# Optimization experiments

Measured on AMD Instinct MI355X. Metric: run time of the kernel, lower is better.

## Reference

```python
import jax, jax.numpy as jnp
import numpy as np

SCAD_A = 3.7
PERCENTILE_Q = 0.75
EPS = 1e-8
LAM_HAT = 0.9
PROP_STEP = 4


def setup_inputs() -> dict:
    key = jax.random.key(0)
    ks = jax.random.split(key, 4)
    N, IN, H, OUT = 4096, 512, 256, 64
    p = 32.0 / N  # avg degree ~32 (pre-symmetrization ~64 after OR, still sparse)
    u = jax.random.uniform(ks[0], (N, N))
    Au = u < p
    Asym = Au | Au.T
    eye = jnp.eye(N, dtype=bool)
    A = jnp.where(eye, 0.0, Asym.astype(jnp.float32))  # zero diagonal; add_loops adds I
    X = jax.random.normal(ks[1], (N, IN), dtype=jnp.float32)
    W1 = jax.random.normal(ks[2], (IN, H), dtype=jnp.float32) / np.sqrt(IN)
    b1 = jnp.zeros((H,), dtype=jnp.float32)
    W2 = jax.random.normal(ks[3], (H, OUT), dtype=jnp.float32) / np.sqrt(H)
    b2 = jnp.zeros((OUT,), dtype=jnp.float32)
    log_gamma_0 = jnp.asarray(np.log(3.0), dtype=jnp.float32)
    raw_decay = jnp.asarray(np.log(0.85 / 0.15), dtype=jnp.float32)
    raw_alpha_blend = jnp.asarray(0.0, dtype=jnp.float32)  # sigmoid -> 0.5 blend
    return {"A": A, "X": X, "W1": W1, "b1": b1, "W2": W2, "b2": b2,
            "log_gamma_0": log_gamma_0, "raw_decay": raw_decay,
            "raw_alpha_blend": raw_alpha_blend}


def _scad_weight(y, lam, a):
    # SCAD-derived reweighting: 1 for y<=lam, (a*lam - y)/((a-1)*y) in the middle, 0 beyond a*lam.
    y_safe = jnp.maximum(y, EPS)  # avoid inf/nan in unselected branch (forward value unchanged)
    w_mid = (a * lam - y) / ((a - 1.0) * y_safe)
    return jnp.where(y <= lam, 1.0, jnp.where(y <= a * lam, w_mid, 0.0))


def reference(A, X, W1, b1, W2, b2, log_gamma_0, raw_decay, raw_alpha_blend):
    N = A.shape[0]
    eye = jnp.eye(N, dtype=A.dtype)
    Ahat = A + eye                          # add_loops
    D = Ahat.sum(-1)                        # [N]
    D_sq = jnp.sqrt(D)[:, None]             # [N,1]
    A_tilde = Ahat / (D_sq * D_sq.T)        # sym_norm: D^{-1/2} A D^{-1/2}
    edge_mask = (Ahat > 0) & (eye == 0)     # A_bool & ~I
    has_edges = edge_mask.sum() > 0

    # MLP (eval mode: dropout inactive)
    F0 = jnp.maximum(X @ W1 + b1, 0.0) @ W2 + b2   # [N, out_dim]

    alpha = jax.nn.sigmoid(raw_alpha_blend)
    g0 = jnp.exp(log_gamma_0)
    r = jax.nn.sigmoid(raw_decay)
    lam = 1.0 / LAM_HAT - 1.0

    Fc = F0
    for k in range(PROP_STEP):
        gamma_param_k = g0 * (r ** k)
        Fn = Fc / D_sq
        nrm = jnp.linalg.norm(Fn, axis=-1, keepdims=True)
        Fu = Fn / jnp.maximum(nrm, EPS)     # F.normalize semantics
        y = jnp.clip(1.0 - Fu @ Fu.T, 0.0, 2.0)  # [N,N] cosine distance
        y = jax.lax.stop_gradient(y)        # y.detach()
        y_edges = jnp.where(edge_mask, y, jnp.nan)
        gamma_data_k = jnp.nanquantile(y_edges, PERCENTILE_Q)
        gamma_data_k = jnp.maximum(jnp.where(has_edges, gamma_data_k, 1.0), EPS)
        lam_combined = alpha * (gamma_param_k / SCAD_A) + (1.0 - alpha) * (gamma_data_k / SCAD_A)
        W = _scad_weight(y, lam_combined, SCAD_A)
        W = W * (1.0 - eye)
        W = jnp.where(jnp.isnan(W), 1.0, W)
        Q_hat = ((W * Ahat).sum(-1) / D + lam)[:, None]
        Fc = (W * A_tilde) @ Fc / Q_hat + lam * F0 / Q_hat
    return Fc
```

## Files before the change

### kernel.cpp

```cpp
#include <hip/hip_runtime.h>
#include <hip/hip_cooperative_groups.h>
#include <math.h>

namespace cg = cooperative_groups;

#define N_NODES 4096
#define IN_DIM  512
#define H_DIM   256
#define OUT_DIM 64
#define SCAD_Af 3.7f
#define EPSf    1e-8f
#define NBINS   2048
#define MAXD    256
#define KSPLIT  4
#define KS_MG   2

__device__ __forceinline__ float scad_w(float y, float lamc) {
    if (y <= lamc) return 1.0f;
    if (y <= SCAD_Af * lamc)
        return (SCAD_Af * lamc - y) / ((SCAD_Af - 1.0f) * fmaxf(y, EPSf));
    return 0.0f;
}

__global__ __launch_bounds__(256, 4)
void k_mega(const float* __restrict__ A,  const float* __restrict__ X,
            const float* __restrict__ W1, const float* __restrict__ b1,
            const float* __restrict__ W2, const float* __restrict__ b2,
            const float* __restrict__ lg0, const float* __restrict__ rdec,
            const float* __restrict__ ralpha,
            int* __restrict__ colIdx, int* __restrict__ rowcnt,
            float* __restrict__ D, float* __restrict__ isD,
            float* __restrict__ Fu, float* __restrict__ part,
            float* __restrict__ F0, float* __restrict__ FcA,
            float* __restrict__ FcB, float* __restrict__ outp,
            unsigned int* __restrict__ hist01) {
    cg::grid_group grid = cg::this_grid();
    const int tid = threadIdx.x;
    const int blk = blockIdx.x;
    const int gid = blk * 256 + tid;
    const int w = tid >> 6, lane = tid & 63;

    __shared__ union {
        struct { float As[16][68]; float Bs[16][64]; } g;
        unsigned int hl[NBINS];
        unsigned int psum[256];
        struct { float h[4][H_DIM]; float w2[64][64]; } m;
    } sm;
    __shared__ float y_loc[4][MAXD];
    __shared__ float vv[2];
    __shared__ float sh_scal;
    __shared__ int   sh_nE;
    __shared__ int   cnt4[4];

    if (blk < 512) {
        int bz = blk >> 8, rem = blk & 255;
        int bx = rem & 3, by = rem >> 2;
        int tx = tid & 15, ty = tid >> 4;
        int bm = by * 64, bn = bx * 64;
        int kbeg = bz * (IN_DIM / KS_MG);
        float acc[4][4] = {};
        for (int k0 = kbeg; k0 < kbeg + IN_DIM / KS_MG; k0 += 16) {
            {
                int r = tid >> 2, kv = tid & 3;
                float4 v = *(const float4*)(X + (size_t)(bm + r) * IN_DIM + k0 + kv * 4);
                sm.g.As[kv * 4 + 0][r] = v.x;
                sm.g.As[kv * 4 + 1][r] = v.y;
                sm.g.As[kv * 4 + 2][r] = v.z;
                sm.g.As[kv * 4 + 3][r] = v.w;
            }
            {
                int kk = tid >> 4, nv = tid & 15;
                *(float4*)&sm.g.Bs[kk][nv * 4] =
                    *(const float4*)(W1 + (size_t)(k0 + kk) * H_DIM + bn + nv * 4);
            }
            __syncthreads();
#pragma unroll
            for (int kk = 0; kk < 16; kk++) {
                float a[4], b[4];
#pragma unroll
                for (int u = 0; u < 4; u++) { a[u] = sm.g.As[kk][ty * 4 + u]; b[u] = sm.g.Bs[kk][tx * 4 + u]; }
#pragma unroll
                for (int u = 0; u < 4; u++)
#pragma unroll
                    for (int v = 0; v < 4; v++) acc[u][v] += a[u] * b[v];
            }
            __syncthreads();
        }
        float* Cm = part + (size_t)bz * N_NODES * H_DIM;
#pragma unroll
        for (int u = 0; u < 4; u++) {
            int m2 = bm + ty * 4 + u;
#pragma unroll
            for (int v = 0; v < 4; v++)
                Cm[(size_t)m2 * H_DIM + bn + tx * 4 + v] = acc[u][v];
        }
    } else {
        int bb = blk - 512;
        int gid2 = bb * 256 + tid;
        if (gid2 < 2 * NBINS) hist01[gid2] = 0u;
#pragma unroll
        for (int rr = 0; rr < 2; rr++) {
            int i = bb * 8 + rr * 4 + w;
            if (lane == 0) cnt4[w] = 0;
            const float4* row4 = (const float4*)(A + (size_t)i * N_NODES);
            int* ci = colIdx + i * MAXD;
            for (int v = lane; v < N_NODES / 4; v += 64) {
                float4 x = row4[v];
                int j0 = v * 4;
                if (x.x != 0.0f) { int p = atomicAdd(&cnt4[w], 1); ci[p] = j0; }
                if (x.y != 0.0f) { int p = atomicAdd(&cnt4[w], 1); ci[p] = j0 + 1; }
                if (x.z != 0.0f) { int p = atomicAdd(&cnt4[w], 1); ci[p] = j0 + 2; }
                if (x.w != 0.0f) { int p = atomicAdd(&cnt4[w], 1); ci[p] = j0 + 3; }
            }
            if (lane == 0) {
                int t = cnt4[w];
                rowcnt[i] = t;
                float d = (float)t + 1.0f;
                D[i] = d;
                isD[i] = 1.0f / sqrtf(d);
            }
        }
    }
    grid.sync();

    {
        unsigned int s = 0;
        for (int q = tid; q < N_NODES; q += 256) s += (unsigned int)rowcnt[q];
        sm.psum[tid] = s;
        __syncthreads();
        for (int off = 128; off; off >>= 1) {
            if (tid < off) sm.psum[tid] += sm.psum[tid + off];
            __syncthreads();
        }
        if (tid == 0) sh_nE = (int)sm.psum[0];
        __syncthreads();

        int i = blk * 4 + w;
        const size_t tot = (size_t)N_NODES * H_DIM;
        const float* p0 = part + (size_t)i * H_DIM;
#pragma unroll
        for (int q = 0; q < 4; q++) {
            int k = q * 64 + lane;
            float s2 = p0[k] + p0[tot + k] + b1[k];
            sm.m.h[w][k] = fmaxf(s2, 0.0f);
        }
        float a0 = 0, a1 = 0, a2 = 0, a3 = 0;
        for (int k0 = 0; k0 < H_DIM; k0 += 64) {
            __syncthreads();
            const float4* src = (const float4*)(W2 + (size_t)k0 * OUT_DIM);
#pragma unroll
            for (int q = 0; q < 4; q++)
                ((float4*)sm.m.w2)[q * 256 + tid] = src[q * 256 + tid];
            __syncthreads();
#pragma unroll 16
            for (int kk = 0; kk < 64; kk += 4) {
                a0 += sm.m.h[w][k0 + kk + 0] * sm.m.w2[kk + 0][lane];
                a1 += sm.m.h[w][k0 + kk + 1] * sm.m.w2[kk + 1][lane];
                a2 += sm.m.h[w][k0 + kk + 2] * sm.m.w2[kk + 2][lane];
                a3 += sm.m.h[w][k0 + kk + 3] * sm.m.w2[kk + 3][lane];
            }
        }
        float f0 = (a0 + a1) + (a2 + a3) + b2[lane];
        F0[(size_t)i * 64 + lane] = f0;
        float fn = f0 * isD[i];
        float s2 = fn * fn;
        for (int off = 32; off; off >>= 1) s2 += __shfl_xor(s2, off, 64);
        Fu[(size_t)i * 64 + lane] = fn / fmaxf(sqrtf(s2), EPSf);
    }
    grid.sync();

    const float lam = (float)(1.0 / 0.9 - 1.0);
    const int eg = lane >> 2, el = lane & 3;
    const int i = blk * 4 + w, c = lane;
    const float* fin = F0;
    for (int k = 0; k < 4; k++) {
        float* fout = (k == 0) ? FcA : (k == 1) ? FcB : (k == 2) ? FcA : outp;
        unsigned int* histK    = hist01 + (k & 1) * NBINS;
        unsigned int* histNext = hist01 + ((k + 1) & 1) * NBINS;

        for (int b = tid; b < NBINS; b += 256) sm.hl[b] = 0u;
        __syncthreads();
        {
            int deg = rowcnt[i];
            const float4* Fu4 = (const float4*)Fu;
            float4 fi0 = Fu4[i * 16 + el * 4 + 0];
            float4 fi1 = Fu4[i * 16 + el * 4 + 1];
            float4 fi2 = Fu4[i * 16 + el * 4 + 2];
            float4 fi3 = Fu4[i * 16 + el * 4 + 3];
            for (int base = 0; base < deg; base += 16) {
                int e = base + eg;
                bool act = e < deg;
                int j = act ? colIdx[i * MAXD + e] : i;
                float4 a0 = Fu4[(size_t)j * 16 + el * 4 + 0];
                float4 a1 = Fu4[(size_t)j * 16 + el * 4 + 1];
                float4 a2 = Fu4[(size_t)j * 16 + el * 4 + 2];
                float4 a3 = Fu4[(size_t)j * 16 + el * 4 + 3];
                float s = fi0.x * a0.x + fi0.y * a0.y + fi0.z * a0.z + fi0.w * a0.w
                        + fi1.x * a1.x + fi1.y * a1.y + fi1.z * a1.z + fi1.w * a1.w
                        + fi2.x * a2.x + fi2.y * a2.y + fi2.z * a2.z + fi2.w * a2.w
                        + fi3.x * a3.x + fi3.y * a3.y + fi3.z * a3.z + fi3.w * a3.w;
                s += __shfl_xor(s, 1, 64);
                s += __shfl_xor(s, 2, 64);
                if (act && el == 0) {
                    float y = 1.0f - s;
                    y = fminf(fmaxf(y, 0.0f), 2.0f);
                    y_loc[w][e] = y;
                    int bin = (int)(y * (NBINS * 0.5f));
                    if (bin > NBINS - 1) bin = NBINS - 1;
                    atomicAdd(&sm.hl[bin], 1u);
                }
            }
        }
        __syncthreads();
        for (int b = tid; b < NBINS; b += 256) {
            unsigned int v = sm.hl[b];
            if (v) atomicAdd(&histK[b], v);
        }
        if (tid < 4 && blk * 4 + tid < NBINS) {}
        if (gid < NBINS) histNext[gid] = 0u;
        grid.sync();

        {
            unsigned int cnt[8];
            const uint4* h4 = (const uint4*)histK;
            unsigned int s = 0;
#pragma unroll
            for (int q = 0; q < 2; q++) {
                uint4 v = h4[tid * 2 + q];
                cnt[q * 4 + 0] = v.x; cnt[q * 4 + 1] = v.y;
                cnt[q * 4 + 2] = v.z; cnt[q * 4 + 3] = v.w;
                s += v.x + v.y + v.z + v.w;
            }
            sm.psum[tid] = s;
            __syncthreads();
            for (int off = 1; off < 256; off <<= 1) {
                unsigned int x = 0;
                if (tid >= off) x = sm.psum[tid - off];
                __syncthreads();
                sm.psum[tid] += x;
                __syncthreads();
            }
            int nE = sh_nE;
            double h = 0.75 * (double)(nE - 1);
            long long i0 = (long long)h;
            float frac = (float)(h - (double)i0);
            unsigned int r0 = (unsigned int)i0, r1 = (unsigned int)(i0 + 1);
            unsigned int cum = (tid == 0) ? 0u : sm.psum[tid - 1];
#pragma unroll
            for (int b = 0; b < 8; b++) {
                unsigned int cn = cnt[b];
                unsigned int lo = cum;
                cum += cn;
                if (cn) {
                    float v = ((float)(tid * 8 + b) + 0.5f) * (2.0f / (float)NBINS);
                    if (lo <= r0 && r0 < cum) vv[0] = v;
                    if (lo <= r1 && r1 < cum) vv[1] = v;
                }
            }
            __syncthreads();
            if (tid == 0) {
                float gd = vv[0] + frac * (vv[1] - vv[0]);
                gd = fmaxf(gd, EPSf);
                float alpha = 1.0f / (1.0f + expf(-ralpha[0]));
                float g0 = expf(lg0[0]);
                float r = 1.0f / (1.0f + expf(-rdec[0]));
                float gp = g0;
                for (int q = 0; q < k; q++) gp *= r;
                sh_scal = alpha * (gp / SCAD_Af) + (1.0f - alpha) * (gd / SCAD_Af);
            }
            __syncthreads();
        }
        {
            float lamc = sh_scal;
            int deg = rowcnt[i];
            float acc = 0.0f, wsum = 0.0f;
            for (int base = 0; base < deg; base += 64) {
                int m = deg - base; if (m > 64) m = 64;
                int   jl = (c < m) ? colIdx[i * MAXD + base + c] : 0;
                float yl = (c < m) ? y_loc[w][base + c] : 9.0f;
                float il = (c < m) ? isD[jl] : 0.0f;
                int tt = 0;
                for (; tt + 4 <= m; tt += 4) {
                    int j0 = __shfl(jl, tt, 64),     j1 = __shfl(jl, tt + 1, 64);
                    int j2 = __shfl(jl, tt + 2, 64), j3 = __shfl(jl, tt + 3, 64);
                    float f0 = fin[(size_t)j0 * 64 + c], f1 = fin[(size_t)j1 * 64 + c];
                    float f2 = fin[(size_t)j2 * 64 + c], f3 = fin[(size_t)j3 * 64 + c];
                    float s0 = scad_w(__shfl(yl, tt, 64),     lamc);
                    float s1 = scad_w(__shfl(yl, tt + 1, 64), lamc);
                    float s2 = scad_w(__shfl(yl, tt + 2, 64), lamc);
                    float s3 = scad_w(__shfl(yl, tt + 3, 64), lamc);
                    wsum += s0 + s1 + s2 + s3;
                    acc += s0 * __shfl(il, tt, 64) * f0 + s1 * __shfl(il, tt + 1, 64) * f1
                         + s2 * __shfl(il, tt + 2, 64) * f2 + s3 * __shfl(il, tt + 3, 64) * f3;
                }
                for (; tt < m; tt++) {
                    int   j = __shfl(jl, tt, 64);
                    float y = __shfl(yl, tt, 64);
                    float wq = scad_w(y, lamc);
                    wsum += wq;
                    acc += wq * __shfl(il, tt, 64) * fin[(size_t)j * 64 + c];
                }
            }
            float Q = wsum / D[i] + lam;
            float fo = (isD[i] * acc + lam * F0[(size_t)i * 64 + c]) / Q;
            fout[(size_t)i * 64 + c] = fo;
            float fn = fo * isD[i];
            float s2n = fn * fn;
            for (int off = 32; off; off >>= 1) s2n += __shfl_xor(s2n, off, 64);
            Fu[(size_t)i * 64 + c] = fn / fmaxf(sqrtf(s2n), EPSf);
        }
        grid.sync();
        fin = fout;
    }
}

__global__ __launch_bounds__(256)
void k_init(const float* __restrict__ A, const float* __restrict__ X,
            const float* __restrict__ W1, float* __restrict__ part,
            int* __restrict__ colIdx, int* __restrict__ rowcnt,
            float* __restrict__ D, float* __restrict__ isD,
            unsigned int* __restrict__ hist01) {
    __shared__ float As[16][68];
    __shared__ float Bs[16][64];
    __shared__ int cnt4[4];
    int tid = threadIdx.x;
    if (blockIdx.x < 1024) {
        int blk = blockIdx.x;
        int bx = blk & 3, by = (blk >> 2) & 63, bz = blk >> 8;
        int tx = tid & 15, ty = tid >> 4;
        int bm = by * 64, bn = bx * 64;
        int kbeg = bz * (IN_DIM / KSPLIT);
        float acc[4][4] = {};
        for (int k0 = kbeg; k0 < kbeg + IN_DIM / KSPLIT; k0 += 16) {
            {
                int r = tid >> 2, kv = tid & 3;
                float4 v = *(const float4*)(X + (size_t)(bm + r) * IN_DIM + k0 + kv * 4);
                As[kv * 4 + 0][r] = v.x;
                As[kv * 4 + 1][r] = v.y;
                As[kv * 4 + 2][r] = v.z;
                As[kv * 4 + 3][r] = v.w;
            }
            {
                int kk = tid >> 4, nv = tid & 15;
                *(float4*)&Bs[kk][nv * 4] =
                    *(const float4*)(W1 + (size_t)(k0 + kk) * H_DIM + bn + nv * 4);
            }
            __syncthreads();
#pragma unroll
            for (int kk = 0; kk < 16; kk++) {
                float a[4], b[4];
#pragma unroll
                for (int u = 0; u < 4; u++) { a[u] = As[kk][ty * 4 + u]; b[u] = Bs[kk][tx * 4 + u]; }
#pragma unroll
                for (int u = 0; u < 4; u++)
#pragma unroll
                    for (int v = 0; v < 4; v++) acc[u][v] += a[u] * b[v];
            }
            __syncthreads();
        }
        float* Cm = part + (size_t)bz * N_NODES * H_DIM;
#pragma unroll
        for (int u = 0; u < 4; u++) {
            int m = bm + ty * 4 + u;
#pragma unroll
            for (int v = 0; v < 4; v++)
                Cm[(size_t)m * H_DIM + bn + tx * 4 + v] = acc[u][v];
        }
    } else {
        int bb = blockIdx.x - 1024;
        int gid2 = bb * 256 + tid;
        if (gid2 < 2 * NBINS) hist01[gid2] = 0u;
        int w = tid >> 6, lane = tid & 63;
        int i = bb * 4 + w;
        if (lane == 0) cnt4[w] = 0;
        __syncthreads();
        const float4* row4 = (const float4*)(A + (size_t)i * N_NODES);
        int* ci = colIdx + i * MAXD;
        for (int v = lane; v < N_NODES / 4; v += 64) {
            float4 x = row4[v];
            int j0 = v * 4;
            if (x.x != 0.0f) { int p = atomicAdd(&cnt4[w], 1); ci[p] = j0; }
            if (x.y != 0.0f) { int p = atomicAdd(&cnt4[w], 1); ci[p] = j0 + 1; }
            if (x.z != 0.0f) { int p = atomicAdd(&cnt4[w], 1); ci[p] = j0 + 2; }
            if (x.w != 0.0f) { int p = atomicAdd(&cnt4[w], 1); ci[p] = j0 + 3; }
        }
        __syncthreads();
        if (lane == 0) {
            int t = cnt4[w];
            rowcnt[i] = t;
            float d = (float)t + 1.0f;
            D[i] = d;
            isD[i] = 1.0f / sqrtf(d);
        }
    }
}

__global__ __launch_bounds__(256)
void k_mlp2(const float* __restrict__ part, const float* __restrict__ b1,
            const float* __restrict__ W2, const float* __restrict__ b2,
            const int* __restrict__ rowcnt, const float* __restrict__ isD,
            float* __restrict__ F0, float* __restrict__ Fu, int* __restrict__ nE) {
    __shared__ float sh_h[4][H_DIM];
    int tid = threadIdx.x;
    if (blockIdx.x == 0) {
        __shared__ unsigned int ps[256];
        unsigned int s = 0;
        for (int q = tid; q < N_NODES; q += 256) s += (unsigned int)rowcnt[q];
        ps[tid] = s;
        __syncthreads();
        for (int off = 128; off; off >>= 1) {
            if (tid < off) ps[tid] += ps[tid + off];
            __syncthreads();
        }
        if (tid == 0) nE[0] = (int)ps[0];
    }
    int w = tid >> 6, lane = tid & 63;
    int i = blockIdx.x * 4 + w;
    const size_t tot = (size_t)N_NODES * H_DIM;
    const float* p0 = part + (size_t)i * H_DIM;
#pragma unroll
    for (int q = 0; q < 4; q++) {
        int k = q * 64 + lane;
        float s = p0[k] + p0[tot + k] + p0[2 * tot + k] + p0[3 * tot + k] + b1[k];
        sh_h[w][k] = fmaxf(s, 0.0f);
    }
    const float* W2c = W2 + lane;
    float a0 = 0, a1 = 0, a2 = 0, a3 = 0;
#pragma unroll 8
    for (int k = 0; k < H_DIM; k += 4) {
        a0 += sh_h[w][k + 0] * W2c[(k + 0) * OUT_DIM];
        a1 += sh_h[w][k + 1] * W2c[(k + 1) * OUT_DIM];
        a2 += sh_h[w][k + 2] * W2c[(k + 2) * OUT_DIM];
        a3 += sh_h[w][k + 3] * W2c[(k + 3) * OUT_DIM];
    }
    float f0 = (a0 + a1) + (a2 + a3) + b2[lane];
    F0[(size_t)i * 64 + lane] = f0;
    float fn = f0 * isD[i];
    float s2 = fn * fn;
    for (int off = 32; off; off >>= 1) s2 += __shfl_xor(s2, off, 64);
    Fu[(size_t)i * 64 + lane] = fn / fmaxf(sqrtf(s2), EPSf);
}

__global__ __launch_bounds__(256)
void k_edgehist(const float* __restrict__ Fu, const int* __restrict__ rowcnt,
                const int* __restrict__ colIdx, float* __restrict__ y_e,
                unsigned int* __restrict__ histK) {
    __shared__ unsigned int hl[NBINS];
    for (int b = threadIdx.x; b < NBINS; b += 256) hl[b] = 0u;
    __syncthreads();
    int gid = blockIdx.x * 256 + threadIdx.x;
    int ri = gid >> 6;
    int lane = threadIdx.x & 63;
    int eg = lane >> 2, el = lane & 3;
    int deg = rowcnt[ri];
    const float4* Fu4 = (const float4*)Fu;
    float4 fi0 = Fu4[ri * 16 + el * 4 + 0];
    float4 fi1 = Fu4[ri * 16 + el * 4 + 1];
    float4 fi2 = Fu4[ri * 16 + el * 4 + 2];
    float4 fi3 = Fu4[ri * 16 + el * 4 + 3];
    for (int base = 0; base < deg; base += 16) {
        int e = base + eg;
        bool act = e < deg;
        int j = act ? colIdx[ri * MAXD + e] : ri;
        float4 a0 = Fu4[(size_t)j * 16 + el * 4 + 0];
        float4 a1 = Fu4[(size_t)j * 16 + el * 4 + 1];
        float4 a2 = Fu4[(size_t)j * 16 + el * 4 + 2];
        float4 a3 = Fu4[(size_t)j * 16 + el * 4 + 3];
        float s = fi0.x * a0.x + fi0.y * a0.y + fi0.z * a0.z + fi0.w * a0.w
                + fi1.x * a1.x + fi1.y * a1.y + fi1.z * a1.z + fi1.w * a1.w
                + fi2.x * a2.x + fi2.y * a2.y + fi2.z * a2.z + fi2.w * a2.w
                + fi3.x * a3.x + fi3.y * a3.y + fi3.z * a3.z + fi3.w * a3.w;
        s += __shfl_xor(s, 1, 64);
        s += __shfl_xor(s, 2, 64);
        if (act && el == 0) {
            float y = 1.0f - s;
            y = fminf(fmaxf(y, 0.0f), 2.0f);
            y_e[ri * MAXD + e] = y;
            int bin = (int)(y * (NBINS * 0.5f));
            if (bin > NBINS - 1) bin = NBINS - 1;
            atomicAdd(&hl[bin], 1u);
        }
    }
    __syncthreads();
    for (int b = threadIdx.x; b < NBINS; b += 256) {
        unsigned int v = hl[b];
        if (v) atomicAdd(&histK[b], v);
    }
}

__global__ __launch_bounds__(256)
void k_propq(const unsigned int* __restrict__ histK, unsigned int* __restrict__ histNext,
             const int* __restrict__ nEp, const int* __restrict__ rowcnt,
             const int* __restrict__ colIdx, const float* __restrict__ y_e,
             const float* __restrict__ Fc, const float* __restrict__ F0,
             const float* __restrict__ D, const float* __restrict__ isD,
             const float* __restrict__ lg0, const float* __restrict__ rdec,
             const float* __restrict__ ralpha, int kiter,
             float* __restrict__ Fout, float* __restrict__ FuNext) {
    __shared__ unsigned int psum[256];
    __shared__ float vv[2];
    __shared__ float sh_scal;
    int tid = threadIdx.x;
    int gid = blockIdx.x * 256 + tid;
    if (gid < NBINS) histNext[gid] = 0u;
    {
        unsigned int cnt[8];
        const uint4* h4 = (const uint4*)histK;
        unsigned int s = 0;
#pragma unroll
        for (int q = 0; q < 2; q++) {
            uint4 v = h4[tid * 2 + q];
            cnt[q * 4 + 0] = v.x; cnt[q * 4 + 1] = v.y;
            cnt[q * 4 + 2] = v.z; cnt[q * 4 + 3] = v.w;
            s += v.x + v.y + v.z + v.w;
        }
        psum[tid] = s;
        __syncthreads();
        for (int off = 1; off < 256; off <<= 1) {
            unsigned int x = 0;
            if (tid >= off) x = psum[tid - off];
            __syncthreads();
            psum[tid] += x;
            __syncthreads();
        }
        int nE = nEp[0];
        double h = 0.75 * (double)(nE - 1);
        long long i0 = (long long)h;
        float frac = (float)(h - (double)i0);
        unsigned int r0 = (unsigned int)i0, r1 = (unsigned int)(i0 + 1);
        unsigned int cum = (tid == 0) ? 0u : psum[tid - 1];
#pragma unroll
        for (int b = 0; b < 8; b++) {
            unsigned int cn = cnt[b];
            unsigned int lo = cum;
            cum += cn;
            if (cn) {
                float v = ((float)(tid * 8 + b) + 0.5f) * (2.0f / (float)NBINS);
                if (lo <= r0 && r0 < cum) vv[0] = v;
                if (lo <= r1 && r1 < cum) vv[1] = v;
            }
        }
        __syncthreads();
        if (tid == 0) {
            float gd = vv[0] + frac * (vv[1] - vv[0]);
            gd = fmaxf(gd, EPSf);
            float alpha = 1.0f / (1.0f + expf(-ralpha[0]));
            float g0 = expf(lg0[0]);
            float r = 1.0f / (1.0f + expf(-rdec[0]));
            float gp = g0;
            for (int q = 0; q < kiter; q++) gp *= r;
            sh_scal = alpha * (gp / SCAD_Af) + (1.0f - alpha) * (gd / SCAD_Af);
        }
        __syncthreads();
    }
    float lamc = sh_scal;
    const float lam = (float)(1.0 / 0.9 - 1.0);
    int i = gid >> 6, c = gid & 63;
    int deg = rowcnt[i];
    float acc = 0.0f, wsum = 0.0f;
    for (int base = 0; base < deg; base += 64) {
        int m = deg - base; if (m > 64) m = 64;
        int   jl = (c < m) ? colIdx[i * MAXD + base + c] : 0;
        float yl = (c < m) ? y_e[i * MAXD + base + c] : 9.0f;
        float il = (c < m) ? isD[jl] : 0.0f;
        int tt = 0;
        for (; tt + 4 <= m; tt += 4) {
            int j0 = __shfl(jl, tt, 64),     j1 = __shfl(jl, tt + 1, 64);
            int j2 = __shfl(jl, tt + 2, 64), j3 = __shfl(jl, tt + 3, 64);
            float f0 = Fc[(size_t)j0 * 64 + c], f1 = Fc[(size_t)j1 * 64 + c];
            float f2 = Fc[(size_t)j2 * 64 + c], f3 = Fc[(size_t)j3 * 64 + c];
            float s0 = scad_w(__shfl(yl, tt, 64),     lamc);
            float s1 = scad_w(__shfl(yl, tt + 1, 64), lamc);
            float s2 = scad_w(__shfl(yl, tt + 2, 64), lamc);
            float s3 = scad_w(__shfl(yl, tt + 3, 64), lamc);
            wsum += s0 + s1 + s2 + s3;
            acc += s0 * __shfl(il, tt, 64) * f0 + s1 * __shfl(il, tt + 1, 64) * f1
                 + s2 * __shfl(il, tt + 2, 64) * f2 + s3 * __shfl(il, tt + 3, 64) * f3;
        }
        for (; tt < m; tt++) {
            int   j = __shfl(jl, tt, 64);
            float y = __shfl(yl, tt, 64);
            float wq = scad_w(y, lamc);
            wsum += wq;
            acc += wq * __shfl(il, tt, 64) * Fc[(size_t)j * 64 + c];
        }
    }
    float Q = wsum / D[i] + lam;
    float fo = (isD[i] * acc + lam * F0[(size_t)i * 64 + c]) / Q;
    Fout[(size_t)i * 64 + c] = fo;
    float fn = fo * isD[i];
    float s2n = fn * fn;
    for (int off = 32; off; off >>= 1) s2n += __shfl_xor(s2n, off, 64);
    FuNext[(size_t)i * 64 + c] = fn / fmaxf(sqrtf(s2n), EPSf);
}

extern "C" void kernel_launch(void* const* d_in, const int* in_sizes, int n_in,
                              void* d_out, int out_size, void* d_ws, size_t ws_size,
                              hipStream_t stream) {
    const float* A      = (const float*)d_in[0];
    const float* X      = (const float*)d_in[1];
    const float* W1     = (const float*)d_in[2];
    const float* b1     = (const float*)d_in[3];
    const float* W2     = (const float*)d_in[4];
    const float* b2     = (const float*)d_in[5];
    const float* lg0    = (const float*)d_in[6];
    const float* rdec   = (const float*)d_in[7];
    const float* ralpha = (const float*)d_in[8];
    float* outp = (float*)d_out;

    char* w = (char*)d_ws;
    size_t off = 0;
    auto carve = [&](size_t bytes) -> char* {
        char* p = w + off;
        off += (bytes + 255) & ~(size_t)255;
        return p;
    };
    int*      colIdx = (int*)carve((size_t)N_NODES * MAXD * 4);
    float*    y_e    = (float*)carve((size_t)N_NODES * MAXD * 4);
    float*    part   = (float*)carve((size_t)KSPLIT * N_NODES * H_DIM * 4);
    int*      rowcnt = (int*)carve(N_NODES * 4);
    float*    D      = (float*)carve(N_NODES * 4);
    float*    isD    = (float*)carve(N_NODES * 4);
    float*    Fu     = (float*)carve((size_t)N_NODES * 64 * 4);
    float*    F0     = (float*)carve((size_t)N_NODES * 64 * 4);
    float*    FcA    = (float*)carve((size_t)N_NODES * 64 * 4);
    float*    FcB    = (float*)carve((size_t)N_NODES * 64 * 4);
    unsigned* hist01 = (unsigned*)carve(2 * NBINS * 4);
    int*      nE     = (int*)carve(256);

    int coopAttr = 0, numCU = 0, maxPerCU = 0;
    (void)hipDeviceGetAttribute(&coopAttr, hipDeviceAttributeCooperativeLaunch, 0);
    (void)hipDeviceGetAttribute(&numCU, hipDeviceAttributeMultiprocessorCount, 0);
    (void)hipOccupancyMaxActiveBlocksPerMultiprocessor(&maxPerCU, k_mega, 256, 0);
    bool useCoop = (coopAttr != 0) && ((long)maxPerCU * (long)numCU >= 1024);

    if (useCoop) {
        void* args[] = {
            (void*)&A, (void*)&X, (void*)&W1, (void*)&b1, (void*)&W2, (void*)&b2,
            (void*)&lg0, (void*)&rdec, (void*)&ralpha,
            (void*)&colIdx, (void*)&rowcnt, (void*)&D, (void*)&isD,
            (void*)&Fu, (void*)&part, (void*)&F0,
            (void*)&FcA, (void*)&FcB, (void*)&outp, (void*)&hist01,
        };
        hipError_t e = hipLaunchCooperativeKernel((void*)k_mega, dim3(1024), dim3(256),
                                                  args, 0, stream);
        if (e == hipSuccess) return;
        (void)hipGetLastError();
    }

    k_init<<<dim3(2048), dim3(256), 0, stream>>>(A, X, W1, part, colIdx, rowcnt, D, isD, hist01);
    k_mlp2<<<dim3(1024), dim3(256), 0, stream>>>(part, b1, W2, b2, rowcnt, isD, F0, Fu, nE);
    const float* fin = F0;
    float* fouts[4] = {FcA, FcB, FcA, outp};
    for (int k = 0; k < 4; k++) {
        unsigned* histK    = hist01 + (k & 1) * NBINS;
        unsigned* histNext = hist01 + ((k + 1) & 1) * NBINS;
        k_edgehist<<<dim3(1024), dim3(256), 0, stream>>>(Fu, rowcnt, colIdx, y_e, histK);
        k_propq<<<dim3(1024), dim3(256), 0, stream>>>(histK, histNext, nE, rowcnt, colIdx,
                                                      y_e, fin, F0, D, isD, lg0, rdec,
                                                      ralpha, k, fouts[k], Fu);
        fin = fouts[k];
    }
}
```

Measured before the change: 307.6 us.

## Fuse first MLP layer per block into mega kernel and drop one grid sync

Removes the split-K tiled X@W1 GEMM phase, which wrote partial sums to global memory and needed a grid-wide barrier before the second layer. Each block now computes its own 4 rows of X@W1 directly, with X staged in shared memory and W1 read by column from global, then applies layer 2. CSR construction moves into the same phase, so one grid.sync and the partial-sum buffer disappear. The trade-off is that every block rereads all of W1 (512x256) from global or L2 with no register tiling, which raises redundant memory traffic in place of the grid barrier.

```diff
diff --git a/kernel.cpp b/kernel.cpp
--- a/kernel.cpp
+++ b/kernel.cpp
@@ -13,7 +13,6 @@
 #define NBINS   2048
 #define MAXD    256
 #define KSPLIT  4
-#define KS_MG   2
 
 __device__ __forceinline__ float scad_w(float y, float lamc) {
     if (y <= lamc) return 1.0f;
@@ -30,10 +29,9 @@
             const float* __restrict__ ralpha,
             int* __restrict__ colIdx, int* __restrict__ rowcnt,
             float* __restrict__ D, float* __restrict__ isD,
-            float* __restrict__ Fu, float* __restrict__ part,
-            float* __restrict__ F0, float* __restrict__ FcA,
-            float* __restrict__ FcB, float* __restrict__ outp,
-            unsigned int* __restrict__ hist01) {
+            float* __restrict__ Fu, float* __restrict__ F0,
+            float* __restrict__ FcA, float* __restrict__ FcB,
+            float* __restrict__ outp, unsigned int* __restrict__ hist01) {
     cg::grid_group grid = cg::this_grid();
     const int tid = threadIdx.x;
     const int blk = blockIdx.x;
@@ -41,10 +39,10 @@
     const int w = tid >> 6, lane = tid & 63;
 
     __shared__ union {
-        struct { float As[16][68]; float Bs[16][64]; } g;
+        float Xs[IN_DIM][4];
+        struct { float h[4][H_DIM]; float w2[64][64]; } m;
         unsigned int hl[NBINS];
         unsigned int psum[256];
-        struct { float h[4][H_DIM]; float w2[64][64]; } m;
     } sm;
     __shared__ float y_loc[4][MAXD];
     __shared__ float vv[2];
@@ -52,98 +50,57 @@
     __shared__ int   sh_nE;
     __shared__ int   cnt4[4];
 
-    if (blk < 512) {
-        int bz = blk >> 8, rem = blk & 255;
-        int bx = rem & 3, by = rem >> 2;
-        int tx = tid & 15, ty = tid >> 4;
-        int bm = by * 64, bn = bx * 64;
-        int kbeg = bz * (IN_DIM / KS_MG);
-        float acc[4][4] = {};
-        for (int k0 = kbeg; k0 < kbeg + IN_DIM / KS_MG; k0 += 16) {
-            {
-                int r = tid >> 2, kv = tid & 3;
-                float4 v = *(const float4*)(X + (size_t)(bm + r) * IN_DIM + k0 + kv * 4);
-                sm.g.As[kv * 4 + 0][r] = v.x;
-                sm.g.As[kv * 4 + 1][r] = v.y;
-                sm.g.As[kv * 4 + 2][r] = v.z;
-                sm.g.As[kv * 4 + 3][r] = v.w;
-            }
-            {
-                int kk = tid >> 4, nv = tid & 15;
-                *(float4*)&sm.g.Bs[kk][nv * 4] =
-                    *(const float4*)(W1 + (size_t)(k0 + kk) * H_DIM + bn + nv * 4);
-            }
-            __syncthreads();
-#pragma unroll
-            for (int kk = 0; kk < 16; kk++) {
-                float a[4], b[4];
-#pragma unroll
-                for (int u = 0; u < 4; u++) { a[u] = sm.g.As[kk][ty * 4 + u]; b[u] = sm.g.Bs[kk][tx * 4 + u]; }
-#pragma unroll
-                for (int u = 0; u < 4; u++)
-#pragma unroll
-                    for (int v = 0; v < 4; v++) acc[u][v] += a[u] * b[v];
-            }
-            __syncthreads();
-        }
-        float* Cm = part + (size_t)bz * N_NODES * H_DIM;
-#pragma unroll
-        for (int u = 0; u < 4; u++) {
-            int m2 = bm + ty * 4 + u;
-#pragma unroll
-            for (int v = 0; v < 4; v++)
-                Cm[(size_t)m2 * H_DIM + bn + tx * 4 + v] = acc[u][v];
-        }
-    } else {
-        int bb = blk - 512;
-        int gid2 = bb * 256 + tid;
-        if (gid2 < 2 * NBINS) hist01[gid2] = 0u;
-#pragma unroll
-        for (int rr = 0; rr < 2; rr++) {
-            int i = bb * 8 + rr * 4 + w;
-            if (lane == 0) cnt4[w] = 0;
-            const float4* row4 = (const float4*)(A + (size_t)i * N_NODES);
-            int* ci = colIdx + i * MAXD;
-            for (int v = lane; v < N_NODES / 4; v += 64) {
-                float4 x = row4[v];
-                int j0 = v * 4;
-                if (x.x != 0.0f) { int p = atomicAdd(&cnt4[w], 1); ci[p] = j0; }
-                if (x.y != 0.0f) { int p = atomicAdd(&cnt4[w], 1); ci[p] = j0 + 1; }
-                if (x.z != 0.0f) { int p = atomicAdd(&cnt4[w], 1); ci[p] = j0 + 2; }
-                if (x.w != 0.0f) { int p = atomicAdd(&cnt4[w], 1); ci[p] = j0 + 3; }
-            }
-            if (lane == 0) {
-                int t = cnt4[w];
-                rowcnt[i] = t;
-                float d = (float)t + 1.0f;
-                D[i] = d;
-                isD[i] = 1.0f / sqrtf(d);
-            }
-        }
-    }
-    grid.sync();
+    const int i = blk * 4 + w;
+    float isd_own;
 
     {
-        unsigned int s = 0;
-        for (int q = tid; q < N_NODES; q += 256) s += (unsigned int)rowcnt[q];
-        sm.psum[tid] = s;
-        __syncthreads();
-        for (int off = 128; off; off >>= 1) {
-            if (tid < off) sm.psum[tid] += sm.psum[tid + off];
-            __syncthreads();
-        }
-        if (tid == 0) sh_nE = (int)sm.psum[0];
-        __syncthreads();
-
-        int i = blk * 4 + w;
-        const size_t tot = (size_t)N_NODES * H_DIM;
-        const float* p0 = part + (size_t)i * H_DIM;
-#pragma unroll
-        for (int q = 0; q < 4; q++) {
-            int k = q * 64 + lane;
-            float s2 = p0[k] + p0[tot + k] + b1[k];
-            sm.m.h[w][k] = fmaxf(s2, 0.0f);
-        }
+        if (gid < 2 * NBINS) hist01[gid] = 0u;
+        if (lane == 0) cnt4[w] = 0;
+        const float4* row4 = (const float4*)(A + (size_t)i * N_NODES);
+        int* ci = colIdx + i * MAXD;
+        for (int v = lane; v < N_NODES / 4; v += 64) {
+            float4 x = row4[v];
+            int j0 = v * 4;
+            if (x.x != 0.0f) { int p = atomicAdd(&cnt4[w], 1); ci[p] = j0; }
+            if (x.y != 0.0f) { int p = atomicAdd(&cnt4[w], 1); ci[p] = j0 + 1; }
+            if (x.z != 0.0f) { int p = atomicAdd(&cnt4[w], 1); ci[p] = j0 + 2; }
+            if (x.w != 0.0f) { int p = atomicAdd(&cnt4[w], 1); ci[p] = j0 + 3; }
+        }
+        int t = cnt4[w];
+        float d = (float)t + 1.0f;
+        isd_own = 1.0f / sqrtf(d);
+        if (lane == 0) {
+            rowcnt[i] = t;
+            D[i] = d;
+            isD[i] = isd_own;
+        }
+    }
+    float h0, h1c, h2, h3;
+    {
+        const float* Xb = X + (size_t)blk * 4 * IN_DIM;
+#pragma unroll
+        for (int it = 0; it < 8; it++) {
+            int idx = it * 256 + tid;
+            int r = idx >> 9, k = idx & (IN_DIM - 1);
+            sm.Xs[k][r] = Xb[(size_t)r * IN_DIM + k];
+        }
+        __syncthreads();
+        float a0 = 0, a1 = 0, a2 = 0, a3 = 0;
+        const float* W1c = W1 + tid;
+#pragma unroll 4
+        for (int k = 0; k < IN_DIM; k++) {
+            float4 xv = *(const float4*)&sm.Xs[k][0];
+            float wv = W1c[(size_t)k * H_DIM];
+            a0 += xv.x * wv; a1 += xv.y * wv; a2 += xv.z * wv; a3 += xv.w * wv;
+        }
+        __syncthreads();
+        float bb = b1[tid];
+        h0 = fmaxf(a0 + bb, 0.0f); h1c = fmaxf(a1 + bb, 0.0f);
+        h2 = fmaxf(a2 + bb, 0.0f); h3 = fmaxf(a3 + bb, 0.0f);
+        sm.m.h[0][tid] = h0; sm.m.h[1][tid] = h1c;
+        sm.m.h[2][tid] = h2; sm.m.h[3][tid] = h3;
+    }
+    {
         float a0 = 0, a1 = 0, a2 = 0, a3 = 0;
         for (int k0 = 0; k0 < H_DIM; k0 += 64) {
             __syncthreads();
@@ -162,16 +119,29 @@
         }
         float f0 = (a0 + a1) + (a2 + a3) + b2[lane];
         F0[(size_t)i * 64 + lane] = f0;
-        float fn = f0 * isD[i];
+        float fn = f0 * isd_own;
         float s2 = fn * fn;
         for (int off = 32; off; off >>= 1) s2 += __shfl_xor(s2, off, 64);
         Fu[(size_t)i * 64 + lane] = fn / fmaxf(sqrtf(s2), EPSf);
     }
     grid.sync();
 
+    {
+        unsigned int s = 0;
+        for (int q = tid; q < N_NODES; q += 256) s += (unsigned int)rowcnt[q];
+        sm.psum[tid] = s;
+        __syncthreads();
+        for (int off = 128; off; off >>= 1) {
+            if (tid < off) sm.psum[tid] += sm.psum[tid + off];
+            __syncthreads();
+        }
+        if (tid == 0) sh_nE = (int)sm.psum[0];
+        __syncthreads();
+    }
+
     const float lam = (float)(1.0 / 0.9 - 1.0);
     const int eg = lane >> 2, el = lane & 3;
-    const int i = blk * 4 + w, c = lane;
+    const int c = lane;
     const float* fin = F0;
     for (int k = 0; k < 4; k++) {
         float* fout = (k == 0) ? FcA : (k == 1) ? FcB : (k == 2) ? FcA : outp;
@@ -216,7 +186,6 @@
             unsigned int v = sm.hl[b];
             if (v) atomicAdd(&histK[b], v);
         }
-        if (tid < 4 && blk * 4 + tid < NBINS) {}
         if (gid < NBINS) histNext[gid] = 0u;
         grid.sync();
 
@@ -302,9 +271,9 @@
                 }
             }
             float Q = wsum / D[i] + lam;
-            float fo = (isD[i] * acc + lam * F0[(size_t)i * 64 + c]) / Q;
+            float fo = (isd_own * acc + lam * F0[(size_t)i * 64 + c]) / Q;
             fout[(size_t)i * 64 + c] = fo;
-            float fn = fo * isD[i];
+            float fn = fo * isd_own;
             float s2n = fn * fn;
             for (int off = 32; off; off >>= 1) s2n += __shfl_xor(s2n, off, 64);
             Fu[(size_t)i * 64 + c] = fn / fmaxf(sqrtf(s2n), EPSf);
@@ -639,7 +608,7 @@
             (void*)&A, (void*)&X, (void*)&W1, (void*)&b1, (void*)&W2, (void*)&b2,
             (void*)&lg0, (void*)&rdec, (void*)&ralpha,
             (void*)&colIdx, (void*)&rowcnt, (void*)&D, (void*)&isD,
-            (void*)&Fu, (void*)&part, (void*)&F0,
+            (void*)&Fu, (void*)&F0,
             (void*)&FcA, (void*)&FcB, (void*)&outp, (void*)&hist01,
         };
         hipError_t e = hipLaunchCooperativeKernel((void*)k_mega, dim3(1024), dim3(256),
```

Result: no change. 309.1 us (+0.5%).
